# Kernel tuning notes

Hardware: AMD Instinct MI355X
Metric: run time of the kernel (lower is better)

## Reference

```python
import jax, jax.numpy as jnp
import numpy as np

P, B, C, H, W = 4, 128, 32, 64, 64
HID = 64


def setup_inputs() -> dict:
    key = jax.random.key(0)
    ks = jax.random.split(key, 8)
    return {
        "x": jax.random.normal(ks[0], (P, B, C, H, W), jnp.float32),
        "conv_w": jax.random.normal(ks[1], (HID, C, 3, 3), jnp.float32) / np.sqrt(C * 9).astype(np.float32),
        "conv_b": jnp.zeros((HID,), jnp.float32),
        "e_w1": jax.random.normal(ks[2], (2 * HID, HID), jnp.float32) / np.sqrt(2 * HID).astype(np.float32),
        "e_b1": jnp.zeros((HID,), jnp.float32),
        "e_w2": jax.random.normal(ks[3], (HID, HID), jnp.float32) / np.sqrt(HID).astype(np.float32),
        "e_b2": jnp.zeros((HID,), jnp.float32),
        "o_w1": jax.random.normal(ks[4], (HID, HID), jnp.float32) / np.sqrt(HID).astype(np.float32),
        "o_b1": jnp.zeros((HID,), jnp.float32),
        "o_w2": jax.random.normal(ks[5], (HID, 1), jnp.float32) / np.sqrt(HID).astype(np.float32),
        "o_b2": jnp.zeros((1,), jnp.float32),
    }


def reference(x, conv_w, conv_b, e_w1, e_b1, e_w2, e_b2, o_w1, o_b1, o_w2, o_b2):
    p, b, c, h, w = x.shape
    # flatten phase and batch dims: [P*B, C, H, W]
    xf = x.reshape(p * b, c, h, w)
    # circular 'same' padding for 3x3 conv, then VALID conv (matches padding_mode='circular')
    xp = jnp.pad(xf, ((0, 0), (0, 0), (1, 1), (1, 1)), mode="wrap")
    y = jax.lax.conv_general_dilated(
        xp, conv_w, window_strides=(1, 1), padding="VALID",
        dimension_numbers=("NCHW", "OIHW", "NCHW"),
    ) + conv_b[None, :, None, None]
    y = jax.nn.relu(y)
    # global average pool -> nodes [B, P, hid]
    nodes = y.mean(axis=(-1, -2)).reshape(p, b, -1).transpose(1, 0, 2)
    hid = nodes.shape[-1]
    # node2edge on a fully-connected P-node graph: edge (i,j) = [node_i(send), node_j(recv)]
    # (equivalent to send_mat @ x, receive_mat @ x with dense one-hot matmuls, done as a gather)
    send = jnp.broadcast_to(nodes[:, :, None, :], (b, p, p, hid))
    recv = jnp.broadcast_to(nodes[:, None, :, :], (b, p, p, hid))
    edges = jnp.concatenate([send, recv], axis=-1)  # [B, P, P, 2*hid]
    e = jax.nn.relu(edges @ e_w1 + e_b1)
    e = jax.nn.relu(e @ e_w2 + e_b2)
    # edge2node: receive_mat.T @ e / P == mean over the send axis
    msg = e.mean(axis=1)  # [B, P, hid]
    o = jax.nn.relu(msg @ o_w1 + o_b1)
    out = jnp.squeeze(o @ o_w2 + o_b2)  # [B, P]
    return out
```

## Files before the change

kernel.cpp:

```cpp
#include <hip/hip_runtime.h>
#include <hip/hip_bf16.h>

typedef unsigned short ushort_t;
typedef __attribute__((ext_vector_type(8))) short short8v;
typedef __attribute__((ext_vector_type(4))) float float4v;

#define NP   4
#define NB   128
#define NIMG 512
#define CIN  32
#define KOUT 64

__device__ __forceinline__ ushort_t f2bf(float f) {
    unsigned u = __float_as_uint(f);
    unsigned r = u + 0x7fffu + ((u >> 16) & 1u);
    return (ushort_t)(r >> 16);
}

__global__ void prep_kernel(const float* __restrict__ conv_w,
                            ushort_t* __restrict__ w_t) {
    int i = blockIdx.x * 256 + threadIdx.x;
    if (i < 9 * KOUT * CIN) {
        int rs  = i >> 11;
        int rem = i & 2047;
        int ko  = rem >> 5;
        int c   = rem & 31;
        w_t[i] = f2bf(conv_w[ko * 288 + c * 9 + rs]);
    }
}

__global__ __launch_bounds__(256, 2)
void conv_pool_kernel(const float* __restrict__ x,
                      const float* __restrict__ conv_b,
                      const ushort_t* __restrict__ w_t,
                      float* __restrict__ partials) {
    __shared__ ushort_t xs[10 * 66 * 32];
    __shared__ float psum[4][64];

    const int tid = threadIdx.x;
    const int n   = blockIdx.x >> 3;
    const int h0  = (blockIdx.x & 7) << 3;
    const long xbase = (long)n * (CIN * 64 * 64);

    for (int u = tid; u < 1280; u += 256) {
        int wq = u & 15;
        int cg = (u >> 4) & 7;
        int lr = u >> 7;
        int gh = (h0 + lr + 63) & 63;
        union { float4 v; float f[4]; } L[4];
        #pragma unroll
        for (int cc = 0; cc < 4; ++cc)
            L[cc].v = *(const float4*)(x + xbase +
                        ((cg * 4 + cc) * 4096 + gh * 64 + wq * 4));
        #pragma unroll
        for (int j = 0; j < 4; ++j) {
            int col  = wq * 4 + 1 + j;
            int cpos = (cg * 4) ^ (((col >> 3) & 3) << 3);
            union { uint2 v; ushort_t s[4]; } t;
            t.s[0] = f2bf(L[0].f[j]); t.s[1] = f2bf(L[1].f[j]);
            t.s[2] = f2bf(L[2].f[j]); t.s[3] = f2bf(L[3].f[j]);
            *(uint2*)&xs[(lr * 66 + col) * 32 + cpos] = t.v;
            if (wq == 0 && j == 0)
                *(uint2*)&xs[(lr * 66 + 65) * 32 + cg * 4] = t.v;
            if (wq == 15 && j == 3)
                *(uint2*)&xs[(lr * 66 + 0) * 32 + cg * 4] = t.v;
        }
    }
    __syncthreads();

    const int lane = tid & 63;
    const int wv   = tid >> 6;
    const int m16  = lane & 15;
    const int q    = lane >> 4;

    int aaddr[8][3];
    #pragma unroll
    for (int mt = 0; mt < 8; ++mt) {
        int lpr = wv * 2 + (mt >> 2);
        int lc  = (mt & 3) * 16 + m16;
        #pragma unroll
        for (int s = 0; s < 3; ++s) {
            int col = lc + s;
            int cr  = (q ^ ((col >> 3) & 3)) << 3;
            aaddr[mt][s] = (lpr * 66 + col) * 32 + cr;
        }
    }

    float4v accv[8][4];
    #pragma unroll
    for (int mt = 0; mt < 8; ++mt)
        #pragma unroll
        for (int nt = 0; nt < 4; ++nt)
            accv[mt][nt] = (float4v){0.f, 0.f, 0.f, 0.f};

    const ushort_t* wt_lane = w_t + (m16 * 32 + (q << 3));

    #pragma unroll
    for (int r = 0; r < 3; ++r) {
        #pragma unroll
        for (int s = 0; s < 3; ++s) {
            const int rs = r * 3 + s;
            short8v bfr[4];
            #pragma unroll
            for (int nt = 0; nt < 4; ++nt)
                bfr[nt] = *(const short8v*)(wt_lane + (rs * 64 + nt * 16) * 32);
            #pragma unroll
            for (int mt = 0; mt < 8; ++mt) {
                short8v afr = *(const short8v*)&xs[aaddr[mt][s] + r * (66 * 32)];
                #pragma unroll
                for (int nt = 0; nt < 4; ++nt)
                    accv[mt][nt] = __builtin_amdgcn_mfma_f32_16x16x32_bf16(
                        afr, bfr[nt], accv[mt][nt], 0, 0, 0);
            }
        }
    }

    float sums[4] = {0.f, 0.f, 0.f, 0.f};
    #pragma unroll
    for (int nt = 0; nt < 4; ++nt) {
        float bias = conv_b[nt * 16 + m16];
        #pragma unroll
        for (int mt = 0; mt < 8; ++mt)
            #pragma unroll
            for (int rg = 0; rg < 4; ++rg)
                sums[nt] += fmaxf(accv[mt][nt][rg] + bias, 0.f);
    }
    #pragma unroll
    for (int nt = 0; nt < 4; ++nt) {
        float sv = sums[nt];
        sv += __shfl_xor(sv, 16);
        sv += __shfl_xor(sv, 32);
        if (lane < 16) psum[wv][nt * 16 + lane] = sv;
    }
    __syncthreads();
    if (tid < 64)
        partials[(long)blockIdx.x * 64 + tid] =
            psum[0][tid] + psum[1][tid] + psum[2][tid] + psum[3][tid];
}

__global__ __launch_bounds__(256)
void mlp_kernel(const float* __restrict__ partials,
                const float* __restrict__ e_w1, const float* __restrict__ e_b1,
                const float* __restrict__ e_w2, const float* __restrict__ e_b2,
                const float* __restrict__ o_w1, const float* __restrict__ o_b1,
                const float* __restrict__ o_w2, const float* __restrict__ o_b2,
                float* __restrict__ out) {
    __shared__ float nodes_s[256], h1s[1024], e2s[1024], msgs[256], o1s[256];

    const int tid = threadIdx.x;
    const int b   = blockIdx.x;

    {
        int p = tid >> 6, h = tid & 63;
        const float* pp = partials + (long)((p * 128 + b) * 8) * 64 + h;
        float s = 0.f;
        #pragma unroll
        for (int hb = 0; hb < 8; ++hb) s += pp[hb * 64];
        nodes_s[tid] = s * (1.f / 4096.f);
    }
    __syncthreads();

    for (int idx = tid; idx < 1024; idx += 256) {
        int e = idx >> 6, h = idx & 63;
        int i_ = e >> 2, j = e & 3;
        float sum = e_b1[h];
        const float* ni = &nodes_s[i_ * 64];
        const float* nj = &nodes_s[j * 64];
        #pragma unroll
        for (int k = 0; k < 64; ++k)
            sum += ni[k] * e_w1[k * 64 + h] + nj[k] * e_w1[(64 + k) * 64 + h];
        h1s[idx] = fmaxf(sum, 0.f);
    }
    __syncthreads();

    for (int idx = tid; idx < 1024; idx += 256) {
        int e = idx >> 6, h = idx & 63;
        float sum = e_b2[h];
        const float* he = &h1s[e * 64];
        #pragma unroll
        for (int k = 0; k < 64; ++k)
            sum += he[k] * e_w2[k * 64 + h];
        e2s[idx] = fmaxf(sum, 0.f);
    }
    __syncthreads();

    {
        int j = tid >> 6, h = tid & 63;
        msgs[tid] = 0.25f * (e2s[(0 * 4 + j) * 64 + h] + e2s[(1 * 4 + j) * 64 + h] +
                             e2s[(2 * 4 + j) * 64 + h] + e2s[(3 * 4 + j) * 64 + h]);
    }
    __syncthreads();

    {
        int j = tid >> 6, h = tid & 63;
        float sum = o_b1[h];
        const float* mj = &msgs[j * 64];
        #pragma unroll
        for (int k = 0; k < 64; ++k)
            sum += mj[k] * o_w1[k * 64 + h];
        o1s[tid] = fmaxf(sum, 0.f);
    }
    __syncthreads();

    {
        const int wv = tid >> 6, lane = tid & 63;
        float v = o1s[wv * 64 + lane] * o_w2[lane];
        v += __shfl_xor(v, 1);
        v += __shfl_xor(v, 2);
        v += __shfl_xor(v, 4);
        v += __shfl_xor(v, 8);
        v += __shfl_xor(v, 16);
        v += __shfl_xor(v, 32);
        if (lane == 0) out[b * 4 + wv] = v + o_b2[0];
    }
}

extern "C" void kernel_launch(void* const* d_in, const int* in_sizes, int n_in,
                              void* d_out, int out_size, void* d_ws, size_t ws_size,
                              hipStream_t stream) {
    const float* x      = (const float*)d_in[0];
    const float* conv_w = (const float*)d_in[1];
    const float* conv_b = (const float*)d_in[2];
    const float* e_w1   = (const float*)d_in[3];
    const float* e_b1   = (const float*)d_in[4];
    const float* e_w2   = (const float*)d_in[5];
    const float* e_b2   = (const float*)d_in[6];
    const float* o_w1   = (const float*)d_in[7];
    const float* o_b1   = (const float*)d_in[8];
    const float* o_w2   = (const float*)d_in[9];
    const float* o_b2   = (const float*)d_in[10];

    float*    partials = (float*)d_ws;
    ushort_t* w_t = (ushort_t*)((char*)d_ws + (size_t)NIMG * 8 * 64 * sizeof(float));

    prep_kernel<<<72, 256, 0, stream>>>(conv_w, w_t);
    conv_pool_kernel<<<NIMG * 8, 256, 0, stream>>>(x, conv_b, w_t, partials);
    mlp_kernel<<<128, 256, 0, stream>>>(partials, e_w1, e_b1, e_w2, e_b2,
                                        o_w1, o_b1, o_w2, o_b2,
                                        (float*)d_out);
}
```

Before: 429.0 us.

## Batch all halo-tile global loads upfront and split MLP across receiver nodes

The conv kernel's staging loop now issues all 20 float4 global loads per thread before any bf16 conversion or LDS store. This raises memory-level parallelism when filling the input tile. The MLP kernel now launches one block per (batch, receiver node) instead of one per batch, giving 512 blocks that each do a quarter of the edge work. The cost is higher register pressure in the conv kernel, which could hurt occupancy under launch_bounds(256,2), and redundant node reductions across MLP blocks.

Measured after the change: 420.1 us (median of 2 runs). 1.02x faster.

```diff
diff --git a/kernel.cpp b/kernel.cpp
--- a/kernel.cpp
+++ b/kernel.cpp
@@ -42,28 +42,38 @@
     const int h0  = (blockIdx.x & 7) << 3;
     const long xbase = (long)n * (CIN * 64 * 64);
 
-    for (int u = tid; u < 1280; u += 256) {
-        int wq = u & 15;
-        int cg = (u >> 4) & 7;
-        int lr = u >> 7;
-        int gh = (h0 + lr + 63) & 63;
-        union { float4 v; float f[4]; } L[4];
-        #pragma unroll
-        for (int cc = 0; cc < 4; ++cc)
-            L[cc].v = *(const float4*)(x + xbase +
-                        ((cg * 4 + cc) * 4096 + gh * 64 + wq * 4));
-        #pragma unroll
-        for (int j = 0; j < 4; ++j) {
-            int col  = wq * 4 + 1 + j;
-            int cpos = (cg * 4) ^ (((col >> 3) & 3) << 3);
-            union { uint2 v; ushort_t s[4]; } t;
-            t.s[0] = f2bf(L[0].f[j]); t.s[1] = f2bf(L[1].f[j]);
-            t.s[2] = f2bf(L[2].f[j]); t.s[3] = f2bf(L[3].f[j]);
-            *(uint2*)&xs[(lr * 66 + col) * 32 + cpos] = t.v;
-            if (wq == 0 && j == 0)
-                *(uint2*)&xs[(lr * 66 + 65) * 32 + cg * 4] = t.v;
-            if (wq == 15 && j == 3)
-                *(uint2*)&xs[(lr * 66 + 0) * 32 + cg * 4] = t.v;
+    {
+        const int wq  = tid & 15;
+        const int cg  = (tid >> 4) & 7;
+        const int lr0 = tid >> 7;
+
+        union F4 { float4 v; float f[4]; };
+        F4 L[5][4];
+        #pragma unroll
+        for (int k = 0; k < 5; ++k) {
+            const int gh = (h0 + lr0 + 2 * k + 63) & 63;
+            #pragma unroll
+            for (int cc = 0; cc < 4; ++cc)
+                L[k][cc].v = *(const float4*)(x + xbase +
+                            ((cg * 4 + cc) * 4096 + gh * 64 + wq * 4));
+        }
+
+        #pragma unroll
+        for (int k = 0; k < 5; ++k) {
+            const int lr = lr0 + 2 * k;
+            #pragma unroll
+            for (int j = 0; j < 4; ++j) {
+                int col  = wq * 4 + 1 + j;
+                int cpos = (cg * 4) ^ (((col >> 3) & 3) << 3);
+                union { uint2 v; ushort_t s[4]; } t;
+                t.s[0] = f2bf(L[k][0].f[j]); t.s[1] = f2bf(L[k][1].f[j]);
+                t.s[2] = f2bf(L[k][2].f[j]); t.s[3] = f2bf(L[k][3].f[j]);
+                *(uint2*)&xs[(lr * 66 + col) * 32 + cpos] = t.v;
+                if (wq == 0 && j == 0)
+                    *(uint2*)&xs[(lr * 66 + 65) * 32 + cg * 4] = t.v;
+                if (wq == 15 && j == 3)
+                    *(uint2*)&xs[(lr * 66 + 0) * 32 + cg * 4] = t.v;
+            }
         }
     }
     __syncthreads();
@@ -145,14 +155,16 @@
                 const float* __restrict__ o_w1, const float* __restrict__ o_b1,
                 const float* __restrict__ o_w2, const float* __restrict__ o_b2,
                 float* __restrict__ out) {
-    __shared__ float nodes_s[256], h1s[1024], e2s[1024], msgs[256], o1s[256];
+    __shared__ float nodes_s[256], h1s[256], e2s[256], msgs[64];
 
     const int tid = threadIdx.x;
-    const int b   = blockIdx.x;
-
-    {
-        int p = tid >> 6, h = tid & 63;
-        const float* pp = partials + (long)((p * 128 + b) * 8) * 64 + h;
+    const int b   = blockIdx.x >> 2;
+    const int j   = blockIdx.x & 3;
+    const int i   = tid >> 6;
+    const int h   = tid & 63;
+
+    {
+        const float* pp = partials + (long)((i * 128 + b) * 8) * 64 + h;
         float s = 0.f;
         #pragma unroll
         for (int hb = 0; hb < 8; ++hb) s += pp[hb * 64];
@@ -160,58 +172,45 @@
     }
     __syncthreads();
 
-    for (int idx = tid; idx < 1024; idx += 256) {
-        int e = idx >> 6, h = idx & 63;
-        int i_ = e >> 2, j = e & 3;
+    {
         float sum = e_b1[h];
-        const float* ni = &nodes_s[i_ * 64];
+        const float* ni = &nodes_s[i * 64];
         const float* nj = &nodes_s[j * 64];
         #pragma unroll
         for (int k = 0; k < 64; ++k)
             sum += ni[k] * e_w1[k * 64 + h] + nj[k] * e_w1[(64 + k) * 64 + h];
-        h1s[idx] = fmaxf(sum, 0.f);
-    }
-    __syncthreads();
-
-    for (int idx = tid; idx < 1024; idx += 256) {
-        int e = idx >> 6, h = idx & 63;
+        h1s[tid] = fmaxf(sum, 0.f);
+    }
+    __syncthreads();
+
+    {
         float sum = e_b2[h];
-        const float* he = &h1s[e * 64];
+        const float* he = &h1s[i * 64];
         #pragma unroll
         for (int k = 0; k < 64; ++k)
             sum += he[k] * e_w2[k * 64 + h];
-        e2s[idx] = fmaxf(sum, 0.f);
-    }
-    __syncthreads();
-
-    {
-        int j = tid >> 6, h = tid & 63;
-        msgs[tid] = 0.25f * (e2s[(0 * 4 + j) * 64 + h] + e2s[(1 * 4 + j) * 64 + h] +
-                             e2s[(2 * 4 + j) * 64 + h] + e2s[(3 * 4 + j) * 64 + h]);
-    }
-    __syncthreads();
-
-    {
-        int j = tid >> 6, h = tid & 63;
-        float sum = o_b1[h];
-        const float* mj = &msgs[j * 64];
+        e2s[tid] = fmaxf(sum, 0.f);
+    }
+    __syncthreads();
+
+    if (tid < 64)
+        msgs[tid] = 0.25f * (e2s[tid] + e2s[64 + tid] +
+                             e2s[128 + tid] + e2s[192 + tid]);
+    __syncthreads();
+
+    if (tid < 64) {
+        float sum = o_b1[tid];
         #pragma unroll
         for (int k = 0; k < 64; ++k)
-            sum += mj[k] * o_w1[k * 64 + h];
-        o1s[tid] = fmaxf(sum, 0.f);
-    }
-    __syncthreads();
-
-    {
-        const int wv = tid >> 6, lane = tid & 63;
-        float v = o1s[wv * 64 + lane] * o_w2[lane];
+            sum += msgs[k] * o_w1[k * 64 + tid];
+        float v = fmaxf(sum, 0.f) * o_w2[tid];
         v += __shfl_xor(v, 1);
         v += __shfl_xor(v, 2);
         v += __shfl_xor(v, 4);
         v += __shfl_xor(v, 8);
         v += __shfl_xor(v, 16);
         v += __shfl_xor(v, 32);
-        if (lane == 0) out[b * 4 + wv] = v + o_b2[0];
+        if (tid == 0) out[b * 4 + j] = v + o_b2[0];
     }
 }
 
@@ -235,7 +234,7 @@
 
     prep_kernel<<<72, 256, 0, stream>>>(conv_w, w_t);
     conv_pool_kernel<<<NIMG * 8, 256, 0, stream>>>(x, conv_b, w_t, partials);
-    mlp_kernel<<<128, 256, 0, stream>>>(partials, e_w1, e_b1, e_w2, e_b2,
-                                        o_w1, o_b1, o_w2, o_b2,
-                                        (float*)d_out);
-}
+    mlp_kernel<<<NB * NP, 256, 0, stream>>>(partials, e_w1, e_b1, e_w2, e_b2,
+                                            o_w1, o_b1, o_w2, o_b2,
+                                            (float*)d_out);
+}
```
